# Kernel tuning notes

Hardware: AMD Instinct MI355X
Metric: run time of the kernel (lower is better)

Reference implementation:

```python
import jax, jax.numpy as jnp
import numpy as np

B, N, D, H, O = 4096, 128, 64, 256, 128  # batch, memory_size, memory_dim, controller_dim, output_size


def setup_inputs() -> dict:
    key = jax.random.key(0)
    ks = jax.random.split(key, 20)
    s = 0.05
    inp = {
        "x": jax.random.normal(ks[0], (B, O), jnp.float32),
        "memory": jax.random.normal(ks[1], (B, N, D), jnp.float32),
        "h": jax.random.normal(ks[2], (B, H), jnp.float32),
        "c": jax.random.normal(ks[3], (B, H), jnp.float32),
        # LSTMCell params (torch layout: gates ordered i, f, g, o; input = x||read_vec of width O+D)
        "W_ih": jax.random.normal(ks[4], (4 * H, O + D), jnp.float32) * s,
        "W_hh": jax.random.normal(ks[5], (4 * H, H), jnp.float32) * s,
        "b_ih": jax.random.normal(ks[6], (4 * H,), jnp.float32) * s,
        "b_hh": jax.random.normal(ks[7], (4 * H,), jnp.float32) * s,
        "W_read": jax.random.normal(ks[8], (N, H), jnp.float32) * s,
        "b_read": jax.random.normal(ks[9], (N,), jnp.float32) * s,
        "W_write": jax.random.normal(ks[10], (N, H), jnp.float32) * s,
        "b_write": jax.random.normal(ks[11], (N,), jnp.float32) * s,
        "W_erase": jax.random.normal(ks[12], (D, H), jnp.float32) * s,
        "b_erase": jax.random.normal(ks[13], (D,), jnp.float32) * s,
        "W_add": jax.random.normal(ks[14], (D, H), jnp.float32) * s,
        "b_add": jax.random.normal(ks[15], (D,), jnp.float32) * s,
        "W_out": jax.random.normal(ks[16], (O, H + D), jnp.float32) * s,
        "b_out": jax.random.normal(ks[17], (O,), jnp.float32) * s,
    }
    return inp


def reference(x, memory, h, c, W_ih, W_hh, b_ih, b_hh, W_read, b_read,
              W_write, b_write, W_erase, b_erase, W_add, b_add, W_out, b_out):
    # read: softmax attention over memory rows, addressed by previous hidden state
    read_w = jax.nn.softmax(h @ W_read.T + b_read, axis=-1)          # [B, N]
    read_vec = jnp.einsum("bn,bnd->bd", read_w, memory)               # [B, D]

    # LSTMCell step (torch gate order: i, f, g, o)
    ctrl_in = jnp.concatenate([x, read_vec], axis=-1)                 # [B, O+D]
    gates = ctrl_in @ W_ih.T + b_ih + h @ W_hh.T + b_hh               # [B, 4H]
    i, f, g, o = jnp.split(gates, 4, axis=-1)
    i, f, o = jax.nn.sigmoid(i), jax.nn.sigmoid(f), jax.nn.sigmoid(o)
    g = jnp.tanh(g)
    c_new = f * c + i * g
    h_new = o * jnp.tanh(c_new)

    # write: outer-product erase/add update
    write_w = jax.nn.softmax(h_new @ W_write.T + b_write, axis=-1)    # [B, N]
    erase = jax.nn.sigmoid(h_new @ W_erase.T + b_erase)               # [B, D]
    add = jnp.tanh(h_new @ W_add.T + b_add)                           # [B, D]
    ww = write_w[:, :, None]                                          # [B, N, 1]
    mem_new = memory * (1.0 - ww * erase[:, None, :]) + ww * add[:, None, :]

    out = jnp.concatenate([h_new, read_vec], axis=-1) @ W_out.T + b_out  # [B, O]
    return (out, mem_new, h_new, c_new)
```

## Files before the change

kernel.cpp:

```cpp
#include <hip/hip_runtime.h>
#include <math.h>


typedef __attribute__((ext_vector_type(8))) short bf16x8;
typedef __attribute__((ext_vector_type(4))) float f32x4;
typedef __attribute__((ext_vector_type(4))) unsigned short us4;

#define MFMA16(a, b, c) __builtin_amdgcn_mfma_f32_16x16x32_bf16(a, b, c, 0, 0, 0)
#define GLL16(gp, lp) __builtin_amdgcn_global_load_lds( \
    (const __attribute__((address_space(1))) void*)(gp), \
    (__attribute__((address_space(3))) void*)(lp), 16, 0, 0)
#define SW(row, s) ((s) ^ ((row) & 3))

__device__ __forceinline__ float sigf(float v) { return 1.f / (1.f + __expf(-v)); }

__device__ __forceinline__ unsigned short f2bf(float f) {
    unsigned u = __builtin_bit_cast(unsigned, f);
    u = (u + 0x7FFFu + ((u >> 16) & 1u)) >> 16;
    return (unsigned short)u;
}

__global__ __launch_bounds__(256) void kA_prep(
    const float* __restrict__ Wih, const float* __restrict__ Whh,
    const float* __restrict__ bih, const float* __restrict__ bhh,
    const float* __restrict__ Wr, const float* __restrict__ br,
    const float* __restrict__ Ww, const float* __restrict__ We,
    const float* __restrict__ Wa, const float* __restrict__ bw,
    const float* __restrict__ be, const float* __restrict__ ba,
    const float* __restrict__ Wo, const float* __restrict__ x,
    const float* __restrict__ h,
    unsigned short* __restrict__ Wg, float* __restrict__ bsum,
    unsigned short* __restrict__ Wh_b, float* __restrict__ bh_b,
    unsigned short* __restrict__ Wo_b, unsigned short* __restrict__ Ag,
    float* __restrict__ read_w)
{
    __shared__ unsigned short As[16 * 32];
    __shared__ unsigned short Bs[128 * 32];
    __shared__ float sc[16][128];

    int t = threadIdx.x;
    int wid = t >> 6, lane = t & 63;
    int cl = lane & 15, ks = lane >> 4;
    int b0 = blockIdx.x * 16;

    int idx = blockIdx.x * 256 + t;
    int stride = gridDim.x * 256;
    for (int i = idx; i < 1024 * 448; i += stride) {
        int r = i / 448, cc = i - r * 448;
        float v = (cc < 192) ? Wih[(size_t)r * 192 + cc] : Whh[(size_t)r * 256 + (cc - 192)];
        Wg[i] = f2bf(v);
    }
    for (int i = idx; i < 1024; i += stride) bsum[i] = bih[i] + bhh[i];
    for (int i = idx; i < 256 * 256; i += stride) {
        int r = i >> 8, cc = i & 255;
        float v = (r < 128) ? Ww[(size_t)r * 256 + cc]
                : (r < 192) ? We[(size_t)(r - 128) * 256 + cc]
                            : Wa[(size_t)(r - 192) * 256 + cc];
        Wh_b[i] = f2bf(v);
    }
    for (int i = idx; i < 256; i += stride)
        bh_b[i] = (i < 128) ? bw[i] : (i < 192 ? be[i - 128] : ba[i - 192]);
    for (int i = idx; i < 128 * 320; i += stride) Wo_b[i] = f2bf(Wo[i]);
    for (int i = idx; i < 4096 * 96; i += stride) {
        int row = i / 96, j = i - row * 96;
        float4 v = (j < 32) ? ((const float4*)(x + (size_t)row * 128))[j]
                            : ((const float4*)(h + (size_t)row * 256))[j - 32];
        us4 o = { f2bf(v.x), f2bf(v.y), f2bf(v.z), f2bf(v.w) };
        int col = (j < 32) ? j * 4 : 192 + (j - 32) * 4;
        *(us4*)(Ag + (size_t)row * 448 + col) = o;
    }

    int aOff = cl * 32 + SW(cl, ks) * 8;
    int bOff[4];
#pragma unroll
    for (int f = 0; f < 4; ++f) {
        int br_ = (wid * 4 + f) * 16 + cl;
        bOff[f] = br_ * 32 + SW(br_, ks) * 8;
    }
    f32x4 acc[4] = {};
    for (int kc = 0; kc < 8; ++kc) {
        __syncthreads();
        {
            int row = t >> 4, k0 = (t & 15) * 2;
            float2 hv = *(const float2*)(h + (size_t)(b0 + row) * 256 + kc * 32 + k0);
            unsigned pk = (unsigned)f2bf(hv.x) | ((unsigned)f2bf(hv.y) << 16);
            *(unsigned*)(As + row * 32 + SW(row, k0 >> 3) * 8 + (k0 & 7)) = pk;
        }
        {
            int row = t >> 1, k0 = (t & 1) * 16;
            const float4* wp = (const float4*)(Wr + (size_t)row * 256 + kc * 32 + k0);
            float4 w0 = wp[0], w1 = wp[1], w2 = wp[2], w3 = wp[3];
            us4 p0 = { f2bf(w0.x), f2bf(w0.y), f2bf(w0.z), f2bf(w0.w) };
            us4 p1 = { f2bf(w1.x), f2bf(w1.y), f2bf(w1.z), f2bf(w1.w) };
            us4 p2 = { f2bf(w2.x), f2bf(w2.y), f2bf(w2.z), f2bf(w2.w) };
            us4 p3 = { f2bf(w3.x), f2bf(w3.y), f2bf(w3.z), f2bf(w3.w) };
            int g0 = k0 >> 3;
            unsigned short* basep = Bs + row * 32;
            *(us4*)(basep + SW(row, g0) * 8)     = p0;
            *(us4*)(basep + SW(row, g0) * 8 + 4) = p1;
            *(us4*)(basep + SW(row, g0 + 1) * 8)     = p2;
            *(us4*)(basep + SW(row, g0 + 1) * 8 + 4) = p3;
        }
        __syncthreads();
        if (wid < 2) {
            bf16x8 a = *(const bf16x8*)(As + aOff);
#pragma unroll
            for (int f = 0; f < 4; ++f)
                acc[f] = MFMA16(a, *(const bf16x8*)(Bs + bOff[f]), acc[f]);
        }
    }
    if (wid < 2) {
#pragma unroll
        for (int f = 0; f < 4; ++f)
#pragma unroll
            for (int r = 0; r < 4; ++r)
                sc[ks * 4 + r][(wid * 4 + f) * 16 + cl] = acc[f][r];
    }
    __syncthreads();
    {
        int row = t >> 4, l = t & 15;
        float v[8];
#pragma unroll
        for (int j = 0; j < 8; ++j) v[j] = sc[row][l + 16 * j] + br[l + 16 * j];
        float m = v[0];
#pragma unroll
        for (int j = 1; j < 8; ++j) m = fmaxf(m, v[j]);
#pragma unroll
        for (int mk = 8; mk >= 1; mk >>= 1) m = fmaxf(m, __shfl_xor(m, mk));
        float s = 0.f;
#pragma unroll
        for (int j = 0; j < 8; ++j) { v[j] = __expf(v[j] - m); s += v[j]; }
#pragma unroll
        for (int mk = 8; mk >= 1; mk >>= 1) s += __shfl_xor(s, mk);
        float inv = 1.f / s;
#pragma unroll
        for (int j = 0; j < 8; ++j)
            read_w[(size_t)(b0 + row) * 128 + l + 16 * j] = v[j] * inv;
    }
}

__global__ __launch_bounds__(256) void k2_read_vec(
    const float* __restrict__ mem, const float* __restrict__ read_w,
    unsigned short* __restrict__ Ag, unsigned short* __restrict__ Aout)
{
    __shared__ float part[16][68];
    int t = threadIdx.x;
    int b = blockIdx.x;
    int np = t >> 4, d4 = t & 15;
    const float4* m4 = (const float4*)(mem + (size_t)b * 8192);
    float4 acc = make_float4(0.f, 0.f, 0.f, 0.f);
#pragma unroll
    for (int j = 0; j < 8; ++j) {
        int n = np + 16 * j;
        float w = read_w[(size_t)b * 128 + n];
        float4 mv = m4[t + 256 * j];
        acc.x += w * mv.x; acc.y += w * mv.y; acc.z += w * mv.z; acc.w += w * mv.w;
    }
    part[np][d4 * 4 + 0] = acc.x; part[np][d4 * 4 + 1] = acc.y;
    part[np][d4 * 4 + 2] = acc.z; part[np][d4 * 4 + 3] = acc.w;
    __syncthreads();
    if (t < 64) {
        float s = 0.f;
#pragma unroll
        for (int q = 0; q < 16; ++q) s += part[q][t];
        unsigned short bv = f2bf(s);
        Ag[(size_t)b * 448 + 128 + t] = bv;
        Aout[(size_t)b * 320 + 256 + t] = bv;
    }
}

__global__ __launch_bounds__(256) void kB_gates(
    const unsigned short* __restrict__ Ag, const unsigned short* __restrict__ Wg,
    const float* __restrict__ bsum, const float* __restrict__ c,
    float* __restrict__ h_new, float* __restrict__ c_new,
    unsigned short* __restrict__ Aout)
{
    __shared__ unsigned short As[64 * 32];
    __shared__ unsigned short Bs[256 * 32];
    int t = threadIdx.x;
    int wid = t >> 6, lane = t & 63;
    int cl = lane & 15, ks = lane >> 4;
    int b0 = blockIdx.x * 64;
    int u0 = blockIdx.y * 64;

    int arow = t >> 2;
    const unsigned short* aSrc = Ag + (size_t)(b0 + arow) * 448 + SW(arow, t & 3) * 8;
    unsigned short* aDst = As + wid * 512;
    const unsigned short* bSrc[4];
    unsigned short* bDst[4];
#pragma unroll
    for (int j = 0; j < 4; ++j) {
        int rl = (j * 256 + t) >> 2;
        int g = rl >> 6, u = rl & 63;
        bSrc[j] = Wg + (size_t)(g * 256 + u0 + u) * 448 + SW(rl, t & 3) * 8;
        bDst[j] = Bs + (j * 256 + wid * 64) * 8;
    }

    int aOff[4];
#pragma unroll
    for (int rf = 0; rf < 4; ++rf) {
        int mr = rf * 16 + cl;
        aOff[rf] = mr * 32 + SW(mr, ks) * 8;
    }
    int bOff[4];
#pragma unroll
    for (int g = 0; g < 4; ++g) {
        int br_ = g * 64 + wid * 16 + cl;
        bOff[g] = br_ * 32 + SW(br_, ks) * 8;
    }

    f32x4 acc[4][4] = {};
    for (int kc = 0; kc < 14; ++kc) {
        __syncthreads();
        GLL16(aSrc, aDst);
        GLL16(bSrc[0], bDst[0]); GLL16(bSrc[1], bDst[1]);
        GLL16(bSrc[2], bDst[2]); GLL16(bSrc[3], bDst[3]);
        aSrc += 32;
#pragma unroll
        for (int j = 0; j < 4; ++j) bSrc[j] += 32;
        __syncthreads();
        bf16x8 a[4], b[4];
#pragma unroll
        for (int rf = 0; rf < 4; ++rf) a[rf] = *(const bf16x8*)(As + aOff[rf]);
#pragma unroll
        for (int g = 0; g < 4; ++g) b[g] = *(const bf16x8*)(Bs + bOff[g]);
#pragma unroll
        for (int rf = 0; rf < 4; ++rf)
#pragma unroll
            for (int g = 0; g < 4; ++g)
                acc[rf][g] = MFMA16(a[rf], b[g], acc[rf][g]);
    }

    int unit = u0 + wid * 16 + cl;
    float bi = bsum[unit], bf_ = bsum[256 + unit];
    float bg = bsum[512 + unit], bo_ = bsum[768 + unit];
#pragma unroll
    for (int rf = 0; rf < 4; ++rf) {
#pragma unroll
        for (int r = 0; r < 4; ++r) {
            int row = b0 + rf * 16 + ks * 4 + r;
            float iv = sigf(acc[rf][0][r] + bi);
            float fv = sigf(acc[rf][1][r] + bf_);
            float gv = tanhf(acc[rf][2][r] + bg);
            float ov = sigf(acc[rf][3][r] + bo_);
            float cv = fv * c[(size_t)row * 256 + unit] + iv * gv;
            float hv = ov * tanhf(cv);
            c_new[(size_t)row * 256 + unit] = cv;
            h_new[(size_t)row * 256 + unit] = hv;
            Aout[(size_t)row * 320 + unit] = f2bf(hv);
        }
    }
}

__global__ __launch_bounds__(256) void kC_heads_out(
    const unsigned short* __restrict__ Aout, const unsigned short* __restrict__ Wh_b,
    const unsigned short* __restrict__ Wo_b, const float* __restrict__ bh_b,
    const float* __restrict__ bo, float* __restrict__ write_w,
    float* __restrict__ erase, float* __restrict__ addv, float* __restrict__ outp)
{
    __shared__ unsigned short As[16 * 32];
    __shared__ unsigned short Bh[256 * 32];
    __shared__ unsigned short Bo[128 * 32];
    __shared__ float sc[16][256];

    int t = threadIdx.x;
    int wid = t >> 6, lane = t & 63;
    int cl = lane & 15, ks = lane >> 4;
    int b0 = blockIdx.x * 16;

    const unsigned short* aSrc = Aout + (size_t)(b0 + (lane >> 2)) * 320 + SW(lane >> 2, lane & 3) * 8;
    const unsigned short* bhSrc[4];
    unsigned short* bhDst[4];
#pragma unroll
    for (int j = 0; j < 4; ++j) {
        int rl = (j * 256 + t) >> 2;
        bhSrc[j] = Wh_b + (size_t)rl * 256 + SW(rl, t & 3) * 8;
        bhDst[j] = Bh + (j * 256 + wid * 64) * 8;
    }
    const unsigned short* boSrc[2];
    unsigned short* boDst[2];
#pragma unroll
    for (int j = 0; j < 2; ++j) {
        int rj = j * 64 + (t >> 2);
        boSrc[j] = Wo_b + (size_t)rj * 320 + SW(rj, t & 3) * 8;
        boDst[j] = Bo + j * 2048 + wid * 512;
    }

    int aOff = cl * 32 + SW(cl, ks) * 8;
    int bOffH[4], bOffO[2];
#pragma unroll
    for (int f = 0; f < 4; ++f) { int br_ = (wid * 4 + f) * 16 + cl; bOffH[f] = br_ * 32 + SW(br_, ks) * 8; }
#pragma unroll
    for (int f = 0; f < 2; ++f) { int br_ = (wid * 2 + f) * 16 + cl; bOffO[f] = br_ * 32 + SW(br_, ks) * 8; }

    f32x4 accH[4] = {};
    f32x4 accO[2] = {};
    for (int kc = 0; kc < 10; ++kc) {
        __syncthreads();
        if (t < 64) GLL16(aSrc, As);
        if (kc < 8) {
            GLL16(bhSrc[0], bhDst[0]); GLL16(bhSrc[1], bhDst[1]);
            GLL16(bhSrc[2], bhDst[2]); GLL16(bhSrc[3], bhDst[3]);
        }
        GLL16(boSrc[0], boDst[0]); GLL16(boSrc[1], boDst[1]);
        aSrc += 32;
#pragma unroll
        for (int j = 0; j < 4; ++j) bhSrc[j] += 32;
#pragma unroll
        for (int j = 0; j < 2; ++j) boSrc[j] += 32;
        __syncthreads();
        bf16x8 a = *(const bf16x8*)(As + aOff);
        if (kc < 8) {
#pragma unroll
            for (int f = 0; f < 4; ++f)
                accH[f] = MFMA16(a, *(const bf16x8*)(Bh + bOffH[f]), accH[f]);
        }
#pragma unroll
        for (int f = 0; f < 2; ++f)
            accO[f] = MFMA16(a, *(const bf16x8*)(Bo + bOffO[f]), accO[f]);
    }

#pragma unroll
    for (int f = 0; f < 4; ++f) {
        int col = (wid * 4 + f) * 16 + cl;
        float bb = bh_b[col];
#pragma unroll
        for (int r = 0; r < 4; ++r)
            sc[ks * 4 + r][col] = accH[f][r] + bb;
    }
#pragma unroll
    for (int f = 0; f < 2; ++f) {
        int col = (wid * 2 + f) * 16 + cl;
        float bb = bo[col];
#pragma unroll
        for (int r = 0; r < 4; ++r)
            outp[(size_t)(b0 + ks * 4 + r) * 128 + col] = accO[f][r] + bb;
    }
    __syncthreads();
    {
        int row = t >> 4, l = t & 15;
        float v[8];
#pragma unroll
        for (int j = 0; j < 8; ++j) v[j] = sc[row][l + 16 * j];
        float m = v[0];
#pragma unroll
        for (int j = 1; j < 8; ++j) m = fmaxf(m, v[j]);
#pragma unroll
        for (int mk = 8; mk >= 1; mk >>= 1) m = fmaxf(m, __shfl_xor(m, mk));
        float s = 0.f;
#pragma unroll
        for (int j = 0; j < 8; ++j) { v[j] = __expf(v[j] - m); s += v[j]; }
#pragma unroll
        for (int mk = 8; mk >= 1; mk >>= 1) s += __shfl_xor(s, mk);
        float inv = 1.f / s;
        int row_g = b0 + row;
#pragma unroll
        for (int j = 0; j < 8; ++j)
            write_w[(size_t)row_g * 128 + l + 16 * j] = v[j] * inv;
#pragma unroll
        for (int j = 0; j < 4; ++j)
            erase[(size_t)row_g * 64 + l + 16 * j] = sigf(sc[row][128 + l + 16 * j]);
#pragma unroll
        for (int j = 0; j < 4; ++j)
            addv[(size_t)row_g * 64 + l + 16 * j] = tanhf(sc[row][192 + l + 16 * j]);
    }
}

__global__ __launch_bounds__(256) void k5_mem_update(
    const float* __restrict__ mem, const float* __restrict__ write_w,
    const float* __restrict__ erase, const float* __restrict__ addv,
    float* __restrict__ mem_new)
{
    int t = threadIdx.x; int b = blockIdx.x;
    int np = t >> 4, d0 = (t & 15) * 4;
    const f32x4* m4 = (const f32x4*)(mem + (size_t)b * 8192);
    f32x4* o4 = (f32x4*)(mem_new + (size_t)b * 8192);
    f32x4 e4 = *(const f32x4*)(erase + (size_t)b * 64 + d0);
    f32x4 a4 = *(const f32x4*)(addv + (size_t)b * 64 + d0);
#pragma unroll
    for (int j = 0; j < 8; ++j) {
        int n = np + 16 * j;
        float w = write_w[(size_t)b * 128 + n];
        f32x4 m = m4[t + 256 * j];
        f32x4 r;
        r[0] = m[0] * (1.f - w * e4[0]) + w * a4[0];
        r[1] = m[1] * (1.f - w * e4[1]) + w * a4[1];
        r[2] = m[2] * (1.f - w * e4[2]) + w * a4[2];
        r[3] = m[3] * (1.f - w * e4[3]) + w * a4[3];
        __builtin_nontemporal_store(r, &o4[t + 256 * j]);
    }
}

extern "C" void kernel_launch(void* const* d_in, const int* in_sizes, int n_in,
                              void* d_out, int out_size, void* d_ws, size_t ws_size,
                              hipStream_t stream)
{
    const float* x    = (const float*)d_in[0];
    const float* mem  = (const float*)d_in[1];
    const float* h    = (const float*)d_in[2];
    const float* c    = (const float*)d_in[3];
    const float* Wih  = (const float*)d_in[4];
    const float* Whh  = (const float*)d_in[5];
    const float* bih  = (const float*)d_in[6];
    const float* bhh  = (const float*)d_in[7];
    const float* Wr   = (const float*)d_in[8];
    const float* br   = (const float*)d_in[9];
    const float* Ww   = (const float*)d_in[10];
    const float* bw   = (const float*)d_in[11];
    const float* We   = (const float*)d_in[12];
    const float* be   = (const float*)d_in[13];
    const float* Wa   = (const float*)d_in[14];
    const float* ba   = (const float*)d_in[15];
    const float* Wo   = (const float*)d_in[16];
    const float* bo   = (const float*)d_in[17];

    float* out     = (float*)d_out;
    float* mem_new = out + 524288;
    float* h_new   = out + 34078720;
    float* c_new   = out + 35127296;

    float* ws      = (float*)d_ws;
    float* read_w  = ws;
    float* write_w = ws + 524288;
    float* erase   = ws + 1048576;
    float* addv    = ws + 1310720;
    float* bsum    = ws + 1572864;
    float* bh_b    = ws + 1573888;
    unsigned short* ub   = (unsigned short*)(ws + 1574144);
    unsigned short* Ag   = ub;
    unsigned short* Aout = ub + 1835008;
    unsigned short* Wg   = ub + 3145728;
    unsigned short* Wh_b = ub + 3604480;
    unsigned short* Wo_b = ub + 3670016;

    kA_prep<<<256, 256, 0, stream>>>(Wih, Whh, bih, bhh, Wr, br, Ww, We, Wa, bw, be, ba,
                                     Wo, x, h, Wg, bsum, Wh_b, bh_b, Wo_b, Ag, read_w);
    k2_read_vec<<<4096, 256, 0, stream>>>(mem, read_w, Ag, Aout);
    kB_gates<<<dim3(64, 4), 256, 0, stream>>>(Ag, Wg, bsum, c, h_new, c_new, Aout);
    kC_heads_out<<<256, 256, 0, stream>>>(Aout, Wh_b, Wo_b, bh_b, bo,
                                          write_w, erase, addv, out);
    k5_mem_update<<<4096, 256, 0, stream>>>(mem, write_w, erase, addv, mem_new);
}
```

Measured before the change: 111.8 us.

## Fuse heads/output GEMM with memory update and move weight packing into read kernel

Moves weight/bias/activation bf16 packing out of the score kernel and into the memory-streaming read kernel, so the prep work overlaps the memory-bound pass. The heads/output GEMM is fused with the erase/add memory update, which keeps write weights, erase and add vectors in LDS instead of a workspace round trip and removes one launch. The gates kernel tile is halved to 32 rows to double the grid. The fused kernel processes 4 rows per block, which wastes most of each MFMA tile and reloads the head weights 1024 times, in exchange for eliminating intermediates.

```diff
diff --git a/kernel.cpp b/kernel.cpp
--- a/kernel.cpp
+++ b/kernel.cpp
@@ -20,19 +20,13 @@
     return (unsigned short)u;
 }
 
-__global__ __launch_bounds__(256) void kA_prep(
-    const float* __restrict__ Wih, const float* __restrict__ Whh,
-    const float* __restrict__ bih, const float* __restrict__ bhh,
-    const float* __restrict__ Wr, const float* __restrict__ br,
-    const float* __restrict__ Ww, const float* __restrict__ We,
-    const float* __restrict__ Wa, const float* __restrict__ bw,
-    const float* __restrict__ be, const float* __restrict__ ba,
-    const float* __restrict__ Wo, const float* __restrict__ x,
-    const float* __restrict__ h,
-    unsigned short* __restrict__ Wg, float* __restrict__ bsum,
-    unsigned short* __restrict__ Wh_b, float* __restrict__ bh_b,
-    unsigned short* __restrict__ Wo_b, unsigned short* __restrict__ Ag,
-    float* __restrict__ read_w)
+__device__ __forceinline__ int swA(int r, int c) {
+    return r * 320 + (c & ~31) + ((((c >> 3) & 3) ^ (r & 3)) << 3) + (c & 7);
+}
+
+__global__ __launch_bounds__(256) void kA_scores(
+    const float* __restrict__ h, const float* __restrict__ Wr,
+    const float* __restrict__ br, float* __restrict__ read_w)
 {
     __shared__ unsigned short As[16 * 32];
     __shared__ unsigned short Bs[128 * 32];
@@ -42,33 +36,6 @@
     int wid = t >> 6, lane = t & 63;
     int cl = lane & 15, ks = lane >> 4;
     int b0 = blockIdx.x * 16;
-
-    int idx = blockIdx.x * 256 + t;
-    int stride = gridDim.x * 256;
-    for (int i = idx; i < 1024 * 448; i += stride) {
-        int r = i / 448, cc = i - r * 448;
-        float v = (cc < 192) ? Wih[(size_t)r * 192 + cc] : Whh[(size_t)r * 256 + (cc - 192)];
-        Wg[i] = f2bf(v);
-    }
-    for (int i = idx; i < 1024; i += stride) bsum[i] = bih[i] + bhh[i];
-    for (int i = idx; i < 256 * 256; i += stride) {
-        int r = i >> 8, cc = i & 255;
-        float v = (r < 128) ? Ww[(size_t)r * 256 + cc]
-                : (r < 192) ? We[(size_t)(r - 128) * 256 + cc]
-                            : Wa[(size_t)(r - 192) * 256 + cc];
-        Wh_b[i] = f2bf(v);
-    }
-    for (int i = idx; i < 256; i += stride)
-        bh_b[i] = (i < 128) ? bw[i] : (i < 192 ? be[i - 128] : ba[i - 192]);
-    for (int i = idx; i < 128 * 320; i += stride) Wo_b[i] = f2bf(Wo[i]);
-    for (int i = idx; i < 4096 * 96; i += stride) {
-        int row = i / 96, j = i - row * 96;
-        float4 v = (j < 32) ? ((const float4*)(x + (size_t)row * 128))[j]
-                            : ((const float4*)(h + (size_t)row * 256))[j - 32];
-        us4 o = { f2bf(v.x), f2bf(v.y), f2bf(v.z), f2bf(v.w) };
-        int col = (j < 32) ? j * 4 : 192 + (j - 32) * 4;
-        *(us4*)(Ag + (size_t)row * 448 + col) = o;
-    }
 
     int aOff = cl * 32 + SW(cl, ks) * 8;
     int bOff[4];
@@ -96,8 +63,8 @@
             us4 p3 = { f2bf(w3.x), f2bf(w3.y), f2bf(w3.z), f2bf(w3.w) };
             int g0 = k0 >> 3;
             unsigned short* basep = Bs + row * 32;
-            *(us4*)(basep + SW(row, g0) * 8)     = p0;
-            *(us4*)(basep + SW(row, g0) * 8 + 4) = p1;
+            *(us4*)(basep + SW(row, g0) * 8)         = p0;
+            *(us4*)(basep + SW(row, g0) * 8 + 4)     = p1;
             *(us4*)(basep + SW(row, g0 + 1) * 8)     = p2;
             *(us4*)(basep + SW(row, g0 + 1) * 8 + 4) = p3;
         }
@@ -139,13 +106,51 @@
     }
 }
 
-__global__ __launch_bounds__(256) void k2_read_vec(
+__global__ __launch_bounds__(256) void k2_stream_pack(
     const float* __restrict__ mem, const float* __restrict__ read_w,
-    unsigned short* __restrict__ Ag, unsigned short* __restrict__ Aout)
+    const float* __restrict__ x, const float* __restrict__ h,
+    const float* __restrict__ Wih, const float* __restrict__ Whh,
+    const float* __restrict__ bih, const float* __restrict__ bhh,
+    const float* __restrict__ Ww, const float* __restrict__ We,
+    const float* __restrict__ Wa, const float* __restrict__ bw,
+    const float* __restrict__ be, const float* __restrict__ ba,
+    const float* __restrict__ Wo,
+    unsigned short* __restrict__ Wg, unsigned short* __restrict__ Wh_b,
+    unsigned short* __restrict__ Wo_b, float* __restrict__ bsum,
+    float* __restrict__ bh_b, unsigned short* __restrict__ Ag,
+    float* __restrict__ rvf)
 {
     __shared__ float part[16][68];
     int t = threadIdx.x;
     int b = blockIdx.x;
+    unsigned idx = b * 256 + t;
+
+    if (idx < 458752) {
+        int r = idx / 448, cc = idx - r * 448;
+        float v = (cc < 192) ? Wih[(size_t)r * 192 + cc] : Whh[(size_t)r * 256 + (cc - 192)];
+        Wg[idx] = f2bf(v);
+    }
+    if (idx < 65536) {
+        int r = idx >> 8, cc = idx & 255;
+        float v = (r < 128) ? Ww[(size_t)r * 256 + cc]
+                : (r < 192) ? We[(size_t)(r - 128) * 256 + cc]
+                            : Wa[(size_t)(r - 192) * 256 + cc];
+        Wh_b[idx] = f2bf(v);
+    }
+    if (idx < 40960) Wo_b[idx] = f2bf(Wo[idx]);
+    if (idx < 1024)  bsum[idx] = bih[idx] + bhh[idx];
+    if (idx < 256)
+        bh_b[idx] = (idx < 128) ? bw[idx] : (idx < 192 ? be[idx - 128] : ba[idx - 192]);
+
+    if (t < 96) {
+        int j = t;
+        float4 v = (j < 32) ? ((const float4*)(x + (size_t)b * 128))[j]
+                            : ((const float4*)(h + (size_t)b * 256))[j - 32];
+        us4 o = { f2bf(v.x), f2bf(v.y), f2bf(v.z), f2bf(v.w) };
+        int col = (j < 32) ? j * 4 : 192 + (j - 32) * 4;
+        *(us4*)(Ag + (size_t)b * 448 + col) = o;
+    }
+
     int np = t >> 4, d4 = t & 15;
     const float4* m4 = (const float4*)(mem + (size_t)b * 8192);
     float4 acc = make_float4(0.f, 0.f, 0.f, 0.f);
@@ -163,27 +168,25 @@
         float s = 0.f;
 #pragma unroll
         for (int q = 0; q < 16; ++q) s += part[q][t];
-        unsigned short bv = f2bf(s);
-        Ag[(size_t)b * 448 + 128 + t] = bv;
-        Aout[(size_t)b * 320 + 256 + t] = bv;
+        Ag[(size_t)b * 448 + 128 + t] = f2bf(s);
+        rvf[(size_t)b * 64 + t] = s;
     }
 }
 
 __global__ __launch_bounds__(256) void kB_gates(
     const unsigned short* __restrict__ Ag, const unsigned short* __restrict__ Wg,
     const float* __restrict__ bsum, const float* __restrict__ c,
-    float* __restrict__ h_new, float* __restrict__ c_new,
-    unsigned short* __restrict__ Aout)
+    float* __restrict__ h_new, float* __restrict__ c_new)
 {
-    __shared__ unsigned short As[64 * 32];
+    __shared__ unsigned short As[32 * 32];
     __shared__ unsigned short Bs[256 * 32];
     int t = threadIdx.x;
     int wid = t >> 6, lane = t & 63;
     int cl = lane & 15, ks = lane >> 4;
-    int b0 = blockIdx.x * 64;
+    int b0 = blockIdx.x * 32;
     int u0 = blockIdx.y * 64;
 
-    int arow = t >> 2;
+    int arow = (t >> 2) & 31;
     const unsigned short* aSrc = Ag + (size_t)(b0 + arow) * 448 + SW(arow, t & 3) * 8;
     unsigned short* aDst = As + wid * 512;
     const unsigned short* bSrc[4];
@@ -196,9 +199,9 @@
         bDst[j] = Bs + (j * 256 + wid * 64) * 8;
     }
 
-    int aOff[4];
-#pragma unroll
-    for (int rf = 0; rf < 4; ++rf) {
+    int aOff[2];
+#pragma unroll
+    for (int rf = 0; rf < 2; ++rf) {
         int mr = rf * 16 + cl;
         aOff[rf] = mr * 32 + SW(mr, ks) * 8;
     }
@@ -209,23 +212,23 @@
         bOff[g] = br_ * 32 + SW(br_, ks) * 8;
     }
 
-    f32x4 acc[4][4] = {};
+    f32x4 acc[2][4] = {};
     for (int kc = 0; kc < 14; ++kc) {
         __syncthreads();
-        GLL16(aSrc, aDst);
+        if (wid < 2) GLL16(aSrc, aDst);
         GLL16(bSrc[0], bDst[0]); GLL16(bSrc[1], bDst[1]);
         GLL16(bSrc[2], bDst[2]); GLL16(bSrc[3], bDst[3]);
         aSrc += 32;
 #pragma unroll
         for (int j = 0; j < 4; ++j) bSrc[j] += 32;
         __syncthreads();
-        bf16x8 a[4], b[4];
-#pragma unroll
-        for (int rf = 0; rf < 4; ++rf) a[rf] = *(const bf16x8*)(As + aOff[rf]);
+        bf16x8 a[2], b[4];
+#pragma unroll
+        for (int rf = 0; rf < 2; ++rf) a[rf] = *(const bf16x8*)(As + aOff[rf]);
 #pragma unroll
         for (int g = 0; g < 4; ++g) b[g] = *(const bf16x8*)(Bs + bOff[g]);
 #pragma unroll
-        for (int rf = 0; rf < 4; ++rf)
+        for (int rf = 0; rf < 2; ++rf)
 #pragma unroll
             for (int g = 0; g < 4; ++g)
                 acc[rf][g] = MFMA16(a[rf], b[g], acc[rf][g]);
@@ -235,7 +238,7 @@
     float bi = bsum[unit], bf_ = bsum[256 + unit];
     float bg = bsum[512 + unit], bo_ = bsum[768 + unit];
 #pragma unroll
-    for (int rf = 0; rf < 4; ++rf) {
+    for (int rf = 0; rf < 2; ++rf) {
 #pragma unroll
         for (int r = 0; r < 4; ++r) {
             int row = b0 + rf * 16 + ks * 4 + r;
@@ -247,28 +250,37 @@
             float hv = ov * tanhf(cv);
             c_new[(size_t)row * 256 + unit] = cv;
             h_new[(size_t)row * 256 + unit] = hv;
-            Aout[(size_t)row * 320 + unit] = f2bf(hv);
-        }
-    }
-}
-
-__global__ __launch_bounds__(256) void kC_heads_out(
-    const unsigned short* __restrict__ Aout, const unsigned short* __restrict__ Wh_b,
-    const unsigned short* __restrict__ Wo_b, const float* __restrict__ bh_b,
-    const float* __restrict__ bo, float* __restrict__ write_w,
-    float* __restrict__ erase, float* __restrict__ addv, float* __restrict__ outp)
+        }
+    }
+}
+
+__global__ __launch_bounds__(256) void kC5(
+    const float* __restrict__ h_new, const float* __restrict__ rvf,
+    const unsigned short* __restrict__ Wh_b, const unsigned short* __restrict__ Wo_b,
+    const float* __restrict__ bh_b, const float* __restrict__ bo,
+    const float* __restrict__ mem, float* __restrict__ outp,
+    float* __restrict__ mem_new)
 {
-    __shared__ unsigned short As[16 * 32];
+    __shared__ unsigned short As[4 * 320];
     __shared__ unsigned short Bh[256 * 32];
     __shared__ unsigned short Bo[128 * 32];
-    __shared__ float sc[16][256];
+    __shared__ float sc[4][384];
+    __shared__ float wL[4][128];
+    __shared__ __align__(16) float eL[4][64];
+    __shared__ __align__(16) float aL[4][64];
 
     int t = threadIdx.x;
     int wid = t >> 6, lane = t & 63;
     int cl = lane & 15, ks = lane >> 4;
-    int b0 = blockIdx.x * 16;
-
-    const unsigned short* aSrc = Aout + (size_t)(b0 + (lane >> 2)) * 320 + SW(lane >> 2, lane & 3) * 8;
+    int b0 = blockIdx.x * 4;
+
+    for (int i = t; i < 4 * 320; i += 256) {
+        int row = i / 320, col = i - row * 320;
+        float v = (col < 256) ? h_new[(size_t)(b0 + row) * 256 + col]
+                              : rvf[(size_t)(b0 + row) * 64 + (col - 256)];
+        As[swA(row, col)] = f2bf(v);
+    }
+
     const unsigned short* bhSrc[4];
     unsigned short* bhDst[4];
 #pragma unroll
@@ -286,58 +298,57 @@
         boDst[j] = Bo + j * 2048 + wid * 512;
     }
 
-    int aOff = cl * 32 + SW(cl, ks) * 8;
     int bOffH[4], bOffO[2];
 #pragma unroll
-    for (int f = 0; f < 4; ++f) { int br_ = (wid * 4 + f) * 16 + cl; bOffH[f] = br_ * 32 + SW(br_, ks) * 8; }
-#pragma unroll
-    for (int f = 0; f < 2; ++f) { int br_ = (wid * 2 + f) * 16 + cl; bOffO[f] = br_ * 32 + SW(br_, ks) * 8; }
+    for (int j = 0; j < 4; ++j) { int br_ = (wid + 4 * j) * 16 + cl; bOffH[j] = br_ * 32 + SW(br_, ks) * 8; }
+#pragma unroll
+    for (int j = 0; j < 2; ++j) { int br_ = (wid + 4 * j) * 16 + cl; bOffO[j] = br_ * 32 + SW(br_, ks) * 8; }
 
     f32x4 accH[4] = {};
     f32x4 accO[2] = {};
     for (int kc = 0; kc < 10; ++kc) {
         __syncthreads();
-        if (t < 64) GLL16(aSrc, As);
         if (kc < 8) {
             GLL16(bhSrc[0], bhDst[0]); GLL16(bhSrc[1], bhDst[1]);
             GLL16(bhSrc[2], bhDst[2]); GLL16(bhSrc[3], bhDst[3]);
+#pragma unroll
+            for (int j = 0; j < 4; ++j) bhSrc[j] += 32;
         }
         GLL16(boSrc[0], boDst[0]); GLL16(boSrc[1], boDst[1]);
-        aSrc += 32;
-#pragma unroll
-        for (int j = 0; j < 4; ++j) bhSrc[j] += 32;
 #pragma unroll
         for (int j = 0; j < 2; ++j) boSrc[j] += 32;
         __syncthreads();
-        bf16x8 a = *(const bf16x8*)(As + aOff);
+        bf16x8 a = *(const bf16x8*)(As + swA(cl & 3, kc * 32 + ks * 8));
         if (kc < 8) {
 #pragma unroll
-            for (int f = 0; f < 4; ++f)
-                accH[f] = MFMA16(a, *(const bf16x8*)(Bh + bOffH[f]), accH[f]);
-        }
-#pragma unroll
-        for (int f = 0; f < 2; ++f)
-            accO[f] = MFMA16(a, *(const bf16x8*)(Bo + bOffO[f]), accO[f]);
-    }
-
-#pragma unroll
-    for (int f = 0; f < 4; ++f) {
-        int col = (wid * 4 + f) * 16 + cl;
-        float bb = bh_b[col];
-#pragma unroll
-        for (int r = 0; r < 4; ++r)
-            sc[ks * 4 + r][col] = accH[f][r] + bb;
-    }
-#pragma unroll
-    for (int f = 0; f < 2; ++f) {
-        int col = (wid * 2 + f) * 16 + cl;
-        float bb = bo[col];
-#pragma unroll
-        for (int r = 0; r < 4; ++r)
-            outp[(size_t)(b0 + ks * 4 + r) * 128 + col] = accO[f][r] + bb;
+            for (int j = 0; j < 4; ++j)
+                accH[j] = MFMA16(a, *(const bf16x8*)(Bh + bOffH[j]), accH[j]);
+        }
+#pragma unroll
+        for (int j = 0; j < 2; ++j)
+            accO[j] = MFMA16(a, *(const bf16x8*)(Bo + bOffO[j]), accO[j]);
+    }
+
+    if (ks == 0) {
+#pragma unroll
+        for (int j = 0; j < 4; ++j) {
+            int col = (wid + 4 * j) * 16 + cl;
+            float bb = bh_b[col];
+#pragma unroll
+            for (int r = 0; r < 4; ++r) sc[r][col] = accH[j][r] + bb;
+        }
+#pragma unroll
+        for (int j = 0; j < 2; ++j) {
+            int ocol = (wid + 4 * j) * 16 + cl;
+            float bb = bo[ocol];
+#pragma unroll
+            for (int r = 0; r < 4; ++r)
+                outp[(size_t)(b0 + r) * 128 + ocol] = accO[j][r] + bb;
+        }
     }
     __syncthreads();
-    {
+
+    if (t < 64) {
         int row = t >> 4, l = t & 15;
         float v[8];
 #pragma unroll
@@ -353,41 +364,30 @@
 #pragma unroll
         for (int mk = 8; mk >= 1; mk >>= 1) s += __shfl_xor(s, mk);
         float inv = 1.f / s;
-        int row_g = b0 + row;
-#pragma unroll
-        for (int j = 0; j < 8; ++j)
-            write_w[(size_t)row_g * 128 + l + 16 * j] = v[j] * inv;
-#pragma unroll
-        for (int j = 0; j < 4; ++j)
-            erase[(size_t)row_g * 64 + l + 16 * j] = sigf(sc[row][128 + l + 16 * j]);
-#pragma unroll
-        for (int j = 0; j < 4; ++j)
-            addv[(size_t)row_g * 64 + l + 16 * j] = tanhf(sc[row][192 + l + 16 * j]);
-    }
-}
-
-__global__ __launch_bounds__(256) void k5_mem_update(
-    const float* __restrict__ mem, const float* __restrict__ write_w,
-    const float* __restrict__ erase, const float* __restrict__ addv,
-    float* __restrict__ mem_new)
-{
-    int t = threadIdx.x; int b = blockIdx.x;
-    int np = t >> 4, d0 = (t & 15) * 4;
-    const f32x4* m4 = (const f32x4*)(mem + (size_t)b * 8192);
-    f32x4* o4 = (f32x4*)(mem_new + (size_t)b * 8192);
-    f32x4 e4 = *(const f32x4*)(erase + (size_t)b * 64 + d0);
-    f32x4 a4 = *(const f32x4*)(addv + (size_t)b * 64 + d0);
-#pragma unroll
-    for (int j = 0; j < 8; ++j) {
-        int n = np + 16 * j;
-        float w = write_w[(size_t)b * 128 + n];
-        f32x4 m = m4[t + 256 * j];
-        f32x4 r;
-        r[0] = m[0] * (1.f - w * e4[0]) + w * a4[0];
-        r[1] = m[1] * (1.f - w * e4[1]) + w * a4[1];
-        r[2] = m[2] * (1.f - w * e4[2]) + w * a4[2];
-        r[3] = m[3] * (1.f - w * e4[3]) + w * a4[3];
-        __builtin_nontemporal_store(r, &o4[t + 256 * j]);
+#pragma unroll
+        for (int j = 0; j < 8; ++j) wL[row][l + 16 * j] = v[j] * inv;
+#pragma unroll
+        for (int j = 0; j < 4; ++j) eL[row][l + 16 * j] = sigf(sc[row][128 + l + 16 * j]);
+#pragma unroll
+        for (int j = 0; j < 4; ++j) aL[row][l + 16 * j] = tanhf(sc[row][192 + l + 16 * j]);
+    }
+    __syncthreads();
+
+    {
+        int r = wid;
+        const f32x4* m4 = (const f32x4*)(mem + (size_t)(b0 + r) * 8192);
+        f32x4* o4 = (f32x4*)(mem_new + (size_t)(b0 + r) * 8192);
+        f32x4 e4 = *(const f32x4*)&eL[r][(lane & 15) * 4];
+        f32x4 a4 = *(const f32x4*)&aL[r][(lane & 15) * 4];
+        f32x4 one = {1.f, 1.f, 1.f, 1.f};
+#pragma unroll
+        for (int j = 0; j < 32; ++j) {
+            int idx = j * 64 + lane;
+            float w = wL[r][j * 4 + (lane >> 4)];
+            f32x4 m = m4[idx];
+            f32x4 res = m * (one - e4 * w) + a4 * w;
+            __builtin_nontemporal_store(res, &o4[idx]);
+        }
     }
 }
 
@@ -421,23 +421,19 @@
 
     float* ws      = (float*)d_ws;
     float* read_w  = ws;
-    float* write_w = ws + 524288;
-    float* erase   = ws + 1048576;
-    float* addv    = ws + 1310720;
-    float* bsum    = ws + 1572864;
-    float* bh_b    = ws + 1573888;
-    unsigned short* ub   = (unsigned short*)(ws + 1574144);
+    float* bsum    = ws + 524288;
+    float* bh_b    = ws + 525312;
+    float* rvf     = ws + 525568;
+    unsigned short* ub   = (unsigned short*)(ws + 787712);
     unsigned short* Ag   = ub;
-    unsigned short* Aout = ub + 1835008;
-    unsigned short* Wg   = ub + 3145728;
-    unsigned short* Wh_b = ub + 3604480;
-    unsigned short* Wo_b = ub + 3670016;
-
-    kA_prep<<<256, 256, 0, stream>>>(Wih, Whh, bih, bhh, Wr, br, Ww, We, Wa, bw, be, ba,
-                                     Wo, x, h, Wg, bsum, Wh_b, bh_b, Wo_b, Ag, read_w);
-    k2_read_vec<<<4096, 256, 0, stream>>>(mem, read_w, Ag, Aout);
-    kB_gates<<<dim3(64, 4), 256, 0, stream>>>(Ag, Wg, bsum, c, h_new, c_new, Aout);
-    kC_heads_out<<<256, 256, 0, stream>>>(Aout, Wh_b, Wo_b, bh_b, bo,
-                                          write_w, erase, addv, out);
-    k5_mem_update<<<4096, 256, 0, stream>>>(mem, write_w, erase, addv, mem_new);
-}
+    unsigned short* Wg   = ub + 1835008;
+    unsigned short* Wh_b = ub + 2293760;
+    unsigned short* Wo_b = ub + 2359296;
+
+    kA_scores<<<256, 256, 0, stream>>>(h, Wr, br, read_w);
+    k2_stream_pack<<<4096, 256, 0, stream>>>(mem, read_w, x, h, Wih, Whh, bih, bhh,
+                                             Ww, We, Wa, bw, be, ba, Wo,
+                                             Wg, Wh_b, Wo_b, bsum, bh_b, Ag, rvf);
+    kB_gates<<<dim3(128, 4), 256, 0, stream>>>(Ag, Wg, bsum, c, h_new, c_new);
+    kC5<<<1024, 256, 0, stream>>>(h_new, rvf, Wh_b, Wo_b, bh_b, bo, mem, out, mem_new);
+}
```

New measurement: 109.2 us. -2.4%, faster.

## Move weight/input packing into the memory-streaming kernel and halve gate tile rows

Applied to the files above, without the earlier changes.

Weight and activation bf16 packing moves out of the 256-block score kernel and into the 4096-block read-vector kernel, so it is spread across many more blocks and overlaps with the memory streaming. The gate GEMM tile shrinks from 64 to 32 batch rows, doubling the grid to 512 blocks for better CU occupancy, at the cost of more B-tile reloads. Only two warps now issue the A loads. Risks include extra per-block work in the streaming kernel and lower MFMA reuse per block.

```diff
diff --git a/kernel.cpp b/kernel.cpp
--- a/kernel.cpp
+++ b/kernel.cpp
@@ -20,19 +20,9 @@
     return (unsigned short)u;
 }
 
-__global__ __launch_bounds__(256) void kA_prep(
-    const float* __restrict__ Wih, const float* __restrict__ Whh,
-    const float* __restrict__ bih, const float* __restrict__ bhh,
-    const float* __restrict__ Wr, const float* __restrict__ br,
-    const float* __restrict__ Ww, const float* __restrict__ We,
-    const float* __restrict__ Wa, const float* __restrict__ bw,
-    const float* __restrict__ be, const float* __restrict__ ba,
-    const float* __restrict__ Wo, const float* __restrict__ x,
-    const float* __restrict__ h,
-    unsigned short* __restrict__ Wg, float* __restrict__ bsum,
-    unsigned short* __restrict__ Wh_b, float* __restrict__ bh_b,
-    unsigned short* __restrict__ Wo_b, unsigned short* __restrict__ Ag,
-    float* __restrict__ read_w)
+__global__ __launch_bounds__(256) void kA_scores(
+    const float* __restrict__ h, const float* __restrict__ Wr,
+    const float* __restrict__ br, float* __restrict__ read_w)
 {
     __shared__ unsigned short As[16 * 32];
     __shared__ unsigned short Bs[128 * 32];
@@ -42,33 +32,6 @@
     int wid = t >> 6, lane = t & 63;
     int cl = lane & 15, ks = lane >> 4;
     int b0 = blockIdx.x * 16;
-
-    int idx = blockIdx.x * 256 + t;
-    int stride = gridDim.x * 256;
-    for (int i = idx; i < 1024 * 448; i += stride) {
-        int r = i / 448, cc = i - r * 448;
-        float v = (cc < 192) ? Wih[(size_t)r * 192 + cc] : Whh[(size_t)r * 256 + (cc - 192)];
-        Wg[i] = f2bf(v);
-    }
-    for (int i = idx; i < 1024; i += stride) bsum[i] = bih[i] + bhh[i];
-    for (int i = idx; i < 256 * 256; i += stride) {
-        int r = i >> 8, cc = i & 255;
-        float v = (r < 128) ? Ww[(size_t)r * 256 + cc]
-                : (r < 192) ? We[(size_t)(r - 128) * 256 + cc]
-                            : Wa[(size_t)(r - 192) * 256 + cc];
-        Wh_b[i] = f2bf(v);
-    }
-    for (int i = idx; i < 256; i += stride)
-        bh_b[i] = (i < 128) ? bw[i] : (i < 192 ? be[i - 128] : ba[i - 192]);
-    for (int i = idx; i < 128 * 320; i += stride) Wo_b[i] = f2bf(Wo[i]);
-    for (int i = idx; i < 4096 * 96; i += stride) {
-        int row = i / 96, j = i - row * 96;
-        float4 v = (j < 32) ? ((const float4*)(x + (size_t)row * 128))[j]
-                            : ((const float4*)(h + (size_t)row * 256))[j - 32];
-        us4 o = { f2bf(v.x), f2bf(v.y), f2bf(v.z), f2bf(v.w) };
-        int col = (j < 32) ? j * 4 : 192 + (j - 32) * 4;
-        *(us4*)(Ag + (size_t)row * 448 + col) = o;
-    }
 
     int aOff = cl * 32 + SW(cl, ks) * 8;
     int bOff[4];
@@ -96,8 +59,8 @@
             us4 p3 = { f2bf(w3.x), f2bf(w3.y), f2bf(w3.z), f2bf(w3.w) };
             int g0 = k0 >> 3;
             unsigned short* basep = Bs + row * 32;
-            *(us4*)(basep + SW(row, g0) * 8)     = p0;
-            *(us4*)(basep + SW(row, g0) * 8 + 4) = p1;
+            *(us4*)(basep + SW(row, g0) * 8)         = p0;
+            *(us4*)(basep + SW(row, g0) * 8 + 4)     = p1;
             *(us4*)(basep + SW(row, g0 + 1) * 8)     = p2;
             *(us4*)(basep + SW(row, g0 + 1) * 8 + 4) = p3;
         }
@@ -139,13 +102,51 @@
     }
 }
 
-__global__ __launch_bounds__(256) void k2_read_vec(
+__global__ __launch_bounds__(256) void k2_stream_pack(
     const float* __restrict__ mem, const float* __restrict__ read_w,
-    unsigned short* __restrict__ Ag, unsigned short* __restrict__ Aout)
+    const float* __restrict__ x, const float* __restrict__ h,
+    const float* __restrict__ Wih, const float* __restrict__ Whh,
+    const float* __restrict__ bih, const float* __restrict__ bhh,
+    const float* __restrict__ Ww, const float* __restrict__ We,
+    const float* __restrict__ Wa, const float* __restrict__ bw,
+    const float* __restrict__ be, const float* __restrict__ ba,
+    const float* __restrict__ Wo,
+    unsigned short* __restrict__ Wg, unsigned short* __restrict__ Wh_b,
+    unsigned short* __restrict__ Wo_b, float* __restrict__ bsum,
+    float* __restrict__ bh_b, unsigned short* __restrict__ Ag,
+    unsigned short* __restrict__ Aout)
 {
     __shared__ float part[16][68];
     int t = threadIdx.x;
     int b = blockIdx.x;
+    unsigned idx = b * 256 + t;
+
+    if (idx < 458752) {
+        int r = idx / 448, cc = idx - r * 448;
+        float v = (cc < 192) ? Wih[(size_t)r * 192 + cc] : Whh[(size_t)r * 256 + (cc - 192)];
+        Wg[idx] = f2bf(v);
+    }
+    if (idx < 65536) {
+        int r = idx >> 8, cc = idx & 255;
+        float v = (r < 128) ? Ww[(size_t)r * 256 + cc]
+                : (r < 192) ? We[(size_t)(r - 128) * 256 + cc]
+                            : Wa[(size_t)(r - 192) * 256 + cc];
+        Wh_b[idx] = f2bf(v);
+    }
+    if (idx < 40960) Wo_b[idx] = f2bf(Wo[idx]);
+    if (idx < 1024)  bsum[idx] = bih[idx] + bhh[idx];
+    if (idx < 256)
+        bh_b[idx] = (idx < 128) ? bw[idx] : (idx < 192 ? be[idx - 128] : ba[idx - 192]);
+
+    if (t < 96) {
+        int j = t;
+        float4 v = (j < 32) ? ((const float4*)(x + (size_t)b * 128))[j]
+                            : ((const float4*)(h + (size_t)b * 256))[j - 32];
+        us4 o = { f2bf(v.x), f2bf(v.y), f2bf(v.z), f2bf(v.w) };
+        int col = (j < 32) ? j * 4 : 192 + (j - 32) * 4;
+        *(us4*)(Ag + (size_t)b * 448 + col) = o;
+    }
+
     int np = t >> 4, d4 = t & 15;
     const float4* m4 = (const float4*)(mem + (size_t)b * 8192);
     float4 acc = make_float4(0.f, 0.f, 0.f, 0.f);
@@ -175,15 +176,15 @@
     float* __restrict__ h_new, float* __restrict__ c_new,
     unsigned short* __restrict__ Aout)
 {
-    __shared__ unsigned short As[64 * 32];
+    __shared__ unsigned short As[32 * 32];
     __shared__ unsigned short Bs[256 * 32];
     int t = threadIdx.x;
     int wid = t >> 6, lane = t & 63;
     int cl = lane & 15, ks = lane >> 4;
-    int b0 = blockIdx.x * 64;
+    int b0 = blockIdx.x * 32;
     int u0 = blockIdx.y * 64;
 
-    int arow = t >> 2;
+    int arow = (t >> 2) & 31;
     const unsigned short* aSrc = Ag + (size_t)(b0 + arow) * 448 + SW(arow, t & 3) * 8;
     unsigned short* aDst = As + wid * 512;
     const unsigned short* bSrc[4];
@@ -196,9 +197,9 @@
         bDst[j] = Bs + (j * 256 + wid * 64) * 8;
     }
 
-    int aOff[4];
-#pragma unroll
-    for (int rf = 0; rf < 4; ++rf) {
+    int aOff[2];
+#pragma unroll
+    for (int rf = 0; rf < 2; ++rf) {
         int mr = rf * 16 + cl;
         aOff[rf] = mr * 32 + SW(mr, ks) * 8;
     }
@@ -209,23 +210,23 @@
         bOff[g] = br_ * 32 + SW(br_, ks) * 8;
     }
 
-    f32x4 acc[4][4] = {};
+    f32x4 acc[2][4] = {};
     for (int kc = 0; kc < 14; ++kc) {
         __syncthreads();
-        GLL16(aSrc, aDst);
+        if (wid < 2) GLL16(aSrc, aDst);
         GLL16(bSrc[0], bDst[0]); GLL16(bSrc[1], bDst[1]);
         GLL16(bSrc[2], bDst[2]); GLL16(bSrc[3], bDst[3]);
         aSrc += 32;
 #pragma unroll
         for (int j = 0; j < 4; ++j) bSrc[j] += 32;
         __syncthreads();
-        bf16x8 a[4], b[4];
-#pragma unroll
-        for (int rf = 0; rf < 4; ++rf) a[rf] = *(const bf16x8*)(As + aOff[rf]);
+        bf16x8 a[2], b[4];
+#pragma unroll
+        for (int rf = 0; rf < 2; ++rf) a[rf] = *(const bf16x8*)(As + aOff[rf]);
 #pragma unroll
         for (int g = 0; g < 4; ++g) b[g] = *(const bf16x8*)(Bs + bOff[g]);
 #pragma unroll
-        for (int rf = 0; rf < 4; ++rf)
+        for (int rf = 0; rf < 2; ++rf)
 #pragma unroll
             for (int g = 0; g < 4; ++g)
                 acc[rf][g] = MFMA16(a[rf], b[g], acc[rf][g]);
@@ -235,7 +236,7 @@
     float bi = bsum[unit], bf_ = bsum[256 + unit];
     float bg = bsum[512 + unit], bo_ = bsum[768 + unit];
 #pragma unroll
-    for (int rf = 0; rf < 4; ++rf) {
+    for (int rf = 0; rf < 2; ++rf) {
 #pragma unroll
         for (int r = 0; r < 4; ++r) {
             int row = b0 + rf * 16 + ks * 4 + r;
@@ -433,10 +434,11 @@
     unsigned short* Wh_b = ub + 3604480;
     unsigned short* Wo_b = ub + 3670016;
 
-    kA_prep<<<256, 256, 0, stream>>>(Wih, Whh, bih, bhh, Wr, br, Ww, We, Wa, bw, be, ba,
-                                     Wo, x, h, Wg, bsum, Wh_b, bh_b, Wo_b, Ag, read_w);
-    k2_read_vec<<<4096, 256, 0, stream>>>(mem, read_w, Ag, Aout);
-    kB_gates<<<dim3(64, 4), 256, 0, stream>>>(Ag, Wg, bsum, c, h_new, c_new, Aout);
+    kA_scores<<<256, 256, 0, stream>>>(h, Wr, br, read_w);
+    k2_stream_pack<<<4096, 256, 0, stream>>>(mem, read_w, x, h, Wih, Whh, bih, bhh,
+                                             Ww, We, Wa, bw, be, ba, Wo,
+                                             Wg, Wh_b, Wo_b, bsum, bh_b, Ag, Aout);
+    kB_gates<<<dim3(128, 4), 256, 0, stream>>>(Ag, Wg, bsum, c, h_new, c_new, Aout);
     kC_heads_out<<<256, 256, 0, stream>>>(Aout, Wh_b, Wo_b, bh_b, bo,
                                           write_w, erase, addv, out);
     k5_mem_update<<<4096, 256, 0, stream>>>(mem, write_w, erase, addv, mem_new);
```

Result: faster. 105.2 us (-5.9%).
